# Kernel optimization log

Hardware: AMD Instinct MI355X
Metric: run time of the kernel (lower is better)

Reference implementation:

```python
import jax, jax.numpy as jnp
import numpy as np

# Fano plane lines (i, j, k): colonies whose octonion product should close, e_i * e_j ~ e_k
FANO = np.array([[0, 1, 3], [1, 2, 4], [2, 3, 5], [3, 4, 6], [4, 5, 0], [5, 6, 1], [6, 0, 2]], dtype=np.int64)


def _oct_structure():
    """8x8x8 structure constants M with (x*y)_k = sum_ij M[i,j,k] x_i y_j,
    built via Cayley-Dickson doubling of quaternions (true octonion multiply)."""
    def qmul(a, b):
        w1, x1, y1, z1 = a
        w2, x2, y2, z2 = b
        return np.array([
            w1 * w2 - x1 * x2 - y1 * y2 - z1 * z2,
            w1 * x2 + x1 * w2 + y1 * z2 - z1 * y2,
            w1 * y2 - x1 * z2 + y1 * w2 + z1 * x2,
            w1 * z2 + x1 * y2 - y1 * x2 + z1 * w2,
        ])

    def qconj(a):
        return a * np.array([1.0, -1.0, -1.0, -1.0])

    M = np.zeros((8, 8, 8), dtype=np.float32)
    I = np.eye(8, dtype=np.float32)
    for i in range(8):
        for j in range(8):
            a1, a2 = I[i, :4], I[i, 4:]
            b1, b2 = I[j, :4], I[j, 4:]
            c1 = qmul(a1, b1) - qmul(qconj(b2), a2)
            c2 = qmul(b2, a1) + qmul(a2, qconj(b1))
            M[i, j] = np.concatenate([c1, c2])
    return M


_M_NP = _oct_structure()


def setup_inputs() -> dict:
    key = jax.random.key(0)
    k1, = jax.random.split(key, 1)
    B = 1048576
    colony_states = jax.random.normal(k1, (B, 7, 8), dtype=jnp.float32)
    log_sensitivity = jnp.ones((), dtype=jnp.float32)  # nn.Parameter init 1.0
    return {"colony_states": colony_states, "log_sensitivity": log_sensitivity}


def reference(colony_states, log_sensitivity):
    M = jnp.asarray(_M_NP, dtype=colony_states.dtype)  # [8,8,8]
    # F.normalize(p=2, dim=-1): x / max(||x||, 1e-12)
    norm = jnp.maximum(jnp.linalg.norm(colony_states, axis=-1, keepdims=True), 1e-12)
    states = colony_states / norm  # [B,7,8]

    xi = states[:, FANO[:, 0]]  # [B,7,8]
    xj = states[:, FANO[:, 1]]  # [B,7,8]
    xk = states[:, FANO[:, 2]]  # [B,7,8]

    # All 7 Fano-line octonion products in one bilinear contraction
    prod = jnp.einsum('bli,blj,ijk->blk', xi, xj, M)  # [B,7,8]
    total_error = jnp.sum((prod - xk) ** 2, axis=(-1, -2))  # [B]
    avg_error = total_error / 7.0
    phi = -jnp.log(avg_error + 1e-8) * jnp.exp(log_sensitivity)
    return jnp.clip(phi, 0.0, 10.0)
```

## Files before the change

kernel.cpp:

```cpp
#include <hip/hip_runtime.h>
#include <math.h>

__device__ __forceinline__ void qmul(float w1, float x1, float y1, float z1,
                                     float w2, float x2, float y2, float z2,
                                     float& w, float& x, float& y, float& z) {
    w = w1 * w2 - x1 * x2 - y1 * y2 - z1 * z2;
    x = w1 * x2 + x1 * w2 + y1 * z2 - z1 * y2;
    y = w1 * y2 - x1 * z2 + y1 * w2 + z1 * x2;
    z = w1 * z2 + x1 * y2 - y1 * x2 + z1 * w2;
}

__global__ __launch_bounds__(256) void oct_fano_kernel(
    const float* __restrict__ in,
    const float* __restrict__ logs,
    float* __restrict__ out,
    int B) {
    int b = blockIdx.x * 256 + threadIdx.x;
    if (b >= B) return;

    float x[7][8];
    const float4* p = (const float4*)(in + (size_t)b * 56);
#pragma unroll
    for (int k = 0; k < 14; k++) {
        float4 v = p[k];
        int r = k >> 1;
        int c = (k & 1) * 4;
        x[r][c + 0] = v.x;
        x[r][c + 1] = v.y;
        x[r][c + 2] = v.z;
        x[r][c + 3] = v.w;
    }

#pragma unroll
    for (int r = 0; r < 7; r++) {
        float s = 0.f;
#pragma unroll
        for (int c = 0; c < 8; c++) s += x[r][c] * x[r][c];
        float n = fmaxf(sqrtf(s), 1e-12f);
        float inv = 1.0f / n;
#pragma unroll
        for (int c = 0; c < 8; c++) x[r][c] *= inv;
    }

    float total = 0.f;
#pragma unroll
    for (int l = 0; l < 7; l++) {
        const float* a = x[l];
        const float* bb = x[(l + 1) % 7];
        const float* ck = x[(l + 3) % 7];

        float p0, p1, p2, p3, p4, p5, p6, p7;
        float t0, t1, t2, t3;
        qmul(a[0], a[1], a[2], a[3], bb[0], bb[1], bb[2], bb[3], p0, p1, p2, p3);
        qmul(bb[4], -bb[5], -bb[6], -bb[7], a[4], a[5], a[6], a[7], t0, t1, t2, t3);
        p0 -= t0; p1 -= t1; p2 -= t2; p3 -= t3;
        qmul(bb[4], bb[5], bb[6], bb[7], a[0], a[1], a[2], a[3], p4, p5, p6, p7);
        qmul(a[4], a[5], a[6], a[7], bb[0], -bb[1], -bb[2], -bb[3], t0, t1, t2, t3);
        p4 += t0; p5 += t1; p6 += t2; p7 += t3;

        float d0 = p0 - ck[0], d1 = p1 - ck[1], d2 = p2 - ck[2], d3 = p3 - ck[3];
        float d4 = p4 - ck[4], d5 = p5 - ck[5], d6 = p6 - ck[6], d7 = p7 - ck[7];
        total += d0 * d0 + d1 * d1 + d2 * d2 + d3 * d3 +
                 d4 * d4 + d5 * d5 + d6 * d6 + d7 * d7;
    }

    float avg = total * (1.0f / 7.0f);
    float phi = -logf(avg + 1e-8f) * expf(logs[0]);
    phi = fminf(fmaxf(phi, 0.0f), 10.0f);
    out[b] = phi;
}

extern "C" void kernel_launch(void* const* d_in, const int* in_sizes, int n_in,
                              void* d_out, int out_size, void* d_ws, size_t ws_size,
                              hipStream_t stream) {
    const float* states = (const float*)d_in[0];
    const float* logs = (const float*)d_in[1];
    float* out = (float*)d_out;
    int B = in_sizes[0] / 56;
    int blocks = (B + 255) / 256;
    oct_fano_kernel<<<blocks, 256, 0, stream>>>(states, logs, out, B);
}
```

Measured before the change: 312.5 us.

## Coalesce input loads via per-wave LDS transpose with persistent prefetching grid

Each wavefront loads a 64-row tile with fully coalesced float4 reads and stages it through a skewed LDS layout. Each thread then reads its own row back conflict-free. A persistent grid-stride loop prefetches the next tile into registers while the current one is computed. This targets the uncoalesced strided per-thread loads, at the cost of extra registers, LDS, and a capped grid that may limit occupancy.

```diff
diff --git a/kernel.cpp b/kernel.cpp
--- a/kernel.cpp
+++ b/kernel.cpp
@@ -14,60 +14,107 @@
     const float* __restrict__ in,
     const float* __restrict__ logs,
     float* __restrict__ out,
-    int B) {
-    int b = blockIdx.x * 256 + threadIdx.x;
-    if (b >= B) return;
+    int B, int ntiles) {
+    __shared__ __align__(16) float4 lds4[4 * 14 * 64];
 
-    float x[7][8];
-    const float4* p = (const float4*)(in + (size_t)b * 56);
+    const int t = threadIdx.x & 63;
+    const int w = threadIdx.x >> 6;
+    float4* __restrict__ L = &lds4[w * (14 * 64)];
+
+    const int wstride = gridDim.x * 4;
+    int tile = blockIdx.x * 4 + w;
+    const float sens = expf(logs[0]);
+
+    float4 v[14];
+    if (tile < ntiles) {
+        const float4* gp = (const float4*)in + (size_t)tile * 896;
+        int nch = min(64, B - (tile << 6)) * 14;
 #pragma unroll
-    for (int k = 0; k < 14; k++) {
-        float4 v = p[k];
-        int r = k >> 1;
-        int c = (k & 1) * 4;
-        x[r][c + 0] = v.x;
-        x[r][c + 1] = v.y;
-        x[r][c + 2] = v.z;
-        x[r][c + 3] = v.w;
+        for (int i = 0; i < 14; i++) {
+            int g = i * 64 + t;
+            if (g < nch) v[i] = gp[g];
+        }
     }
 
+    while (tile < ntiles) {
+        const int nb = min(64, B - (tile << 6));
+        const int nch = nb * 14;
+
 #pragma unroll
-    for (int r = 0; r < 7; r++) {
-        float s = 0.f;
+        for (int i = 0; i < 14; i++) {
+            int g = i * 64 + t;
+            if (g < nch) {
+                int bg = g / 14;
+                int cg = g - bg * 14;
+                L[cg * 64 + ((bg + cg) & 63)] = v[i];
+            }
+        }
+
+        const int next = tile + wstride;
+        if (next < ntiles) {
+            const float4* gp = (const float4*)in + (size_t)next * 896;
+            int nch2 = min(64, B - (next << 6)) * 14;
 #pragma unroll
-        for (int c = 0; c < 8; c++) s += x[r][c] * x[r][c];
-        float n = fmaxf(sqrtf(s), 1e-12f);
-        float inv = 1.0f / n;
+            for (int i = 0; i < 14; i++) {
+                int g = i * 64 + t;
+                if (g < nch2) v[i] = gp[g];
+            }
+        }
+
+        if (t < nb) {
+            float x[7][8];
 #pragma unroll
-        for (int c = 0; c < 8; c++) x[r][c] *= inv;
+            for (int k = 0; k < 14; k++) {
+                float4 q = L[k * 64 + ((t + k) & 63)];
+                int r = k >> 1;
+                int c = (k & 1) * 4;
+                x[r][c + 0] = q.x;
+                x[r][c + 1] = q.y;
+                x[r][c + 2] = q.z;
+                x[r][c + 3] = q.w;
+            }
+
+#pragma unroll
+            for (int r = 0; r < 7; r++) {
+                float s = 0.f;
+#pragma unroll
+                for (int c = 0; c < 8; c++) s += x[r][c] * x[r][c];
+                float n = fmaxf(sqrtf(s), 1e-12f);
+                float inv = 1.0f / n;
+#pragma unroll
+                for (int c = 0; c < 8; c++) x[r][c] *= inv;
+            }
+
+            float total = 0.f;
+#pragma unroll
+            for (int l = 0; l < 7; l++) {
+                const float* a = x[l];
+                const float* bb = x[(l + 1) % 7];
+                const float* ck = x[(l + 3) % 7];
+
+                float p0, p1, p2, p3, p4, p5, p6, p7;
+                float t0, t1, t2, t3;
+                qmul(a[0], a[1], a[2], a[3], bb[0], bb[1], bb[2], bb[3], p0, p1, p2, p3);
+                qmul(bb[4], -bb[5], -bb[6], -bb[7], a[4], a[5], a[6], a[7], t0, t1, t2, t3);
+                p0 -= t0; p1 -= t1; p2 -= t2; p3 -= t3;
+                qmul(bb[4], bb[5], bb[6], bb[7], a[0], a[1], a[2], a[3], p4, p5, p6, p7);
+                qmul(a[4], a[5], a[6], a[7], bb[0], -bb[1], -bb[2], -bb[3], t0, t1, t2, t3);
+                p4 += t0; p5 += t1; p6 += t2; p7 += t3;
+
+                float d0 = p0 - ck[0], d1 = p1 - ck[1], d2 = p2 - ck[2], d3 = p3 - ck[3];
+                float d4 = p4 - ck[4], d5 = p5 - ck[5], d6 = p6 - ck[6], d7 = p7 - ck[7];
+                total += d0 * d0 + d1 * d1 + d2 * d2 + d3 * d3 +
+                         d4 * d4 + d5 * d5 + d6 * d6 + d7 * d7;
+            }
+
+            float avg = total * (1.0f / 7.0f);
+            float phi = -logf(avg + 1e-8f) * sens;
+            phi = fminf(fmaxf(phi, 0.0f), 10.0f);
+            out[(tile << 6) + t] = phi;
+        }
+
+        tile = next;
     }
-
-    float total = 0.f;
-#pragma unroll
-    for (int l = 0; l < 7; l++) {
-        const float* a = x[l];
-        const float* bb = x[(l + 1) % 7];
-        const float* ck = x[(l + 3) % 7];
-
-        float p0, p1, p2, p3, p4, p5, p6, p7;
-        float t0, t1, t2, t3;
-        qmul(a[0], a[1], a[2], a[3], bb[0], bb[1], bb[2], bb[3], p0, p1, p2, p3);
-        qmul(bb[4], -bb[5], -bb[6], -bb[7], a[4], a[5], a[6], a[7], t0, t1, t2, t3);
-        p0 -= t0; p1 -= t1; p2 -= t2; p3 -= t3;
-        qmul(bb[4], bb[5], bb[6], bb[7], a[0], a[1], a[2], a[3], p4, p5, p6, p7);
-        qmul(a[4], a[5], a[6], a[7], bb[0], -bb[1], -bb[2], -bb[3], t0, t1, t2, t3);
-        p4 += t0; p5 += t1; p6 += t2; p7 += t3;
-
-        float d0 = p0 - ck[0], d1 = p1 - ck[1], d2 = p2 - ck[2], d3 = p3 - ck[3];
-        float d4 = p4 - ck[4], d5 = p5 - ck[5], d6 = p6 - ck[6], d7 = p7 - ck[7];
-        total += d0 * d0 + d1 * d1 + d2 * d2 + d3 * d3 +
-                 d4 * d4 + d5 * d5 + d6 * d6 + d7 * d7;
-    }
-
-    float avg = total * (1.0f / 7.0f);
-    float phi = -logf(avg + 1e-8f) * expf(logs[0]);
-    phi = fminf(fmaxf(phi, 0.0f), 10.0f);
-    out[b] = phi;
 }
 
 extern "C" void kernel_launch(void* const* d_in, const int* in_sizes, int n_in,
@@ -77,6 +124,8 @@
     const float* logs = (const float*)d_in[1];
     float* out = (float*)d_out;
     int B = in_sizes[0] / 56;
-    int blocks = (B + 255) / 256;
-    oct_fano_kernel<<<blocks, 256, 0, stream>>>(states, logs, out, B);
+    int ntiles = (B + 63) / 64;
+    int nblocks = (ntiles + 3) / 4;
+    if (nblocks > 512) nblocks = 512;
+    oct_fano_kernel<<<nblocks, 256, 0, stream>>>(states, logs, out, B, ntiles);
 }
```

New measurement: 428.6 us. +37.1%, slower.

## Stage input tiles through LDS with direct global-to-LDS loads for coalescing

Applied to the files above, without the earlier changes.

The kernel now gives each 64-thread block a tile of 64 batch rows. It copies the tile into shared memory with coalesced 16-byte global_load_lds transfers, and each thread then reads its own 56-float row back from LDS. The aim is to replace the strided per-thread float4 loads, where each thread reads a 224-byte row, with fully contiguous wavefront accesses. The trade-offs are a hand-encoded waitcnt and a block size cut to 64. The LDS reads at stride 14 float4 may also cause bank conflicts.

```diff
diff --git a/kernel.cpp b/kernel.cpp
--- a/kernel.cpp
+++ b/kernel.cpp
@@ -1,5 +1,6 @@
 #include <hip/hip_runtime.h>
 #include <math.h>
+#include <stdint.h>
 
 __device__ __forceinline__ void qmul(float w1, float x1, float y1, float z1,
                                      float w2, float x2, float y2, float z2,
@@ -10,64 +11,84 @@
     z = w1 * z2 + x1 * y2 - y1 * x2 + z1 * w2;
 }
 
-__global__ __launch_bounds__(256) void oct_fano_kernel(
+typedef __attribute__((address_space(3))) uint32_t lds_u32;
+typedef const __attribute__((address_space(1))) uint32_t glb_u32;
+
+__global__ __launch_bounds__(64) void oct_fano_kernel(
     const float* __restrict__ in,
     const float* __restrict__ logs,
     float* __restrict__ out,
     int B) {
-    int b = blockIdx.x * 256 + threadIdx.x;
-    if (b >= B) return;
+    __shared__ __align__(16) float4 lds4[14 * 64];
 
-    float x[7][8];
-    const float4* p = (const float4*)(in + (size_t)b * 56);
+    const int t = threadIdx.x;
+    const int tile = blockIdx.x;
+    const int nb = min(64, B - (tile << 6));
+
+    const float4* gp = (const float4*)in;
+    const long gbase = (long)tile * 896;
+    const long gmax = (long)B * 14 - 1;
 #pragma unroll
-    for (int k = 0; k < 14; k++) {
-        float4 v = p[k];
-        int r = k >> 1;
-        int c = (k & 1) * 4;
-        x[r][c + 0] = v.x;
-        x[r][c + 1] = v.y;
-        x[r][c + 2] = v.z;
-        x[r][c + 3] = v.w;
+    for (int c = 0; c < 14; c++) {
+        long idx = gbase + c * 64 + t;
+        if (idx > gmax) idx = gmax;
+        __builtin_amdgcn_global_load_lds((glb_u32*)(gp + idx),
+                                         (lds_u32*)&lds4[c * 64], 16, 0, 0);
     }
+    __builtin_amdgcn_s_waitcnt(0x0F70);
+    __builtin_amdgcn_sched_barrier(0);
+
+    if (t < nb) {
+        float x[7][8];
+#pragma unroll
+        for (int k = 0; k < 14; k++) {
+            float4 q = lds4[t * 14 + k];
+            int r = k >> 1;
+            int c = (k & 1) * 4;
+            x[r][c + 0] = q.x;
+            x[r][c + 1] = q.y;
+            x[r][c + 2] = q.z;
+            x[r][c + 3] = q.w;
+        }
 
 #pragma unroll
-    for (int r = 0; r < 7; r++) {
-        float s = 0.f;
+        for (int r = 0; r < 7; r++) {
+            float s = 0.f;
 #pragma unroll
-        for (int c = 0; c < 8; c++) s += x[r][c] * x[r][c];
-        float n = fmaxf(sqrtf(s), 1e-12f);
-        float inv = 1.0f / n;
+            for (int c = 0; c < 8; c++) s += x[r][c] * x[r][c];
+            float n = fmaxf(sqrtf(s), 1e-12f);
+            float inv = 1.0f / n;
 #pragma unroll
-        for (int c = 0; c < 8; c++) x[r][c] *= inv;
+            for (int c = 0; c < 8; c++) x[r][c] *= inv;
+        }
+
+        float total = 0.f;
+#pragma unroll
+        for (int l = 0; l < 7; l++) {
+            const float* a = x[l];
+            const float* bb = x[(l + 1) % 7];
+            const float* ck = x[(l + 3) % 7];
+
+            float p0, p1, p2, p3, p4, p5, p6, p7;
+            float t0, t1, t2, t3;
+            qmul(a[0], a[1], a[2], a[3], bb[0], bb[1], bb[2], bb[3], p0, p1, p2, p3);
+            qmul(bb[4], -bb[5], -bb[6], -bb[7], a[4], a[5], a[6], a[7], t0, t1, t2, t3);
+            p0 -= t0; p1 -= t1; p2 -= t2; p3 -= t3;
+            qmul(bb[4], bb[5], bb[6], bb[7], a[0], a[1], a[2], a[3], p4, p5, p6, p7);
+            qmul(a[4], a[5], a[6], a[7], bb[0], -bb[1], -bb[2], -bb[3], t0, t1, t2, t3);
+            p4 += t0; p5 += t1; p6 += t2; p7 += t3;
+
+            float d0 = p0 - ck[0], d1 = p1 - ck[1], d2 = p2 - ck[2], d3 = p3 - ck[3];
+            float d4 = p4 - ck[4], d5 = p5 - ck[5], d6 = p6 - ck[6], d7 = p7 - ck[7];
+            total += d0 * d0 + d1 * d1 + d2 * d2 + d3 * d3 +
+                     d4 * d4 + d5 * d5 + d6 * d6 + d7 * d7;
+        }
+
+        float avg = total * (1.0f / 7.0f);
+        float phi = -logf(avg + 1e-8f) * expf(logs[0]);
+        phi = fminf(fmaxf(phi, 0.0f), 10.0f);
+        out[(tile << 6) + t] = phi;
     }
-
-    float total = 0.f;
-#pragma unroll
-    for (int l = 0; l < 7; l++) {
-        const float* a = x[l];
-        const float* bb = x[(l + 1) % 7];
-        const float* ck = x[(l + 3) % 7];
-
-        float p0, p1, p2, p3, p4, p5, p6, p7;
-        float t0, t1, t2, t3;
-        qmul(a[0], a[1], a[2], a[3], bb[0], bb[1], bb[2], bb[3], p0, p1, p2, p3);
-        qmul(bb[4], -bb[5], -bb[6], -bb[7], a[4], a[5], a[6], a[7], t0, t1, t2, t3);
-        p0 -= t0; p1 -= t1; p2 -= t2; p3 -= t3;
-        qmul(bb[4], bb[5], bb[6], bb[7], a[0], a[1], a[2], a[3], p4, p5, p6, p7);
-        qmul(a[4], a[5], a[6], a[7], bb[0], -bb[1], -bb[2], -bb[3], t0, t1, t2, t3);
-        p4 += t0; p5 += t1; p6 += t2; p7 += t3;
-
-        float d0 = p0 - ck[0], d1 = p1 - ck[1], d2 = p2 - ck[2], d3 = p3 - ck[3];
-        float d4 = p4 - ck[4], d5 = p5 - ck[5], d6 = p6 - ck[6], d7 = p7 - ck[7];
-        total += d0 * d0 + d1 * d1 + d2 * d2 + d3 * d3 +
-                 d4 * d4 + d5 * d5 + d6 * d6 + d7 * d7;
-    }
-
-    float avg = total * (1.0f / 7.0f);
-    float phi = -logf(avg + 1e-8f) * expf(logs[0]);
-    phi = fminf(fmaxf(phi, 0.0f), 10.0f);
-    out[b] = phi;
 }
 
 extern "C" void kernel_launch(void* const* d_in, const int* in_sizes, int n_in,
@@ -77,6 +98,6 @@
     const float* logs = (const float*)d_in[1];
     float* out = (float*)d_out;
     int B = in_sizes[0] / 56;
-    int blocks = (B + 255) / 256;
-    oct_fano_kernel<<<blocks, 256, 0, stream>>>(states, logs, out, B);
+    int ntiles = (B + 63) / 64;
+    oct_fano_kernel<<<ntiles, 64, 0, stream>>>(states, logs, out, B);
 }
```

After: 313.4 us. Within noise of the previous version (+0.3%).
